# Optimization experiments

Hardware: AMD Instinct MI355X
Metric: run time of the kernel (lower is better)

Reference implementation:

```python
import jax, jax.numpy as jnp
import numpy as np

N = 55          # node count hardcoded in the original forward's reshape
IN_CH = 8192    # in_channel
OUT_SZ = 8192   # out_sz
NEG_SLOPE = 0.01  # torch nn.LeakyReLU default


def setup_inputs() -> dict:
    key = jax.random.key(0)
    ks = jax.random.split(key, 8)
    s1 = 1.0 / np.sqrt(IN_CH)
    s2 = 1.0 / np.sqrt(OUT_SZ)
    return {
        "x": jax.random.normal(ks[0], (N, IN_CH), dtype=jnp.float32),
        "adj": jax.random.uniform(ks[1], (N, N), dtype=jnp.float32),       # unused by forward
        "p_covs": jax.random.uniform(ks[2], (N,), dtype=jnp.float32),      # unused by forward
        # conv1: Conv1d(in_channel, out_sz, 1) == per-node linear
        "W1": jax.random.uniform(ks[3], (OUT_SZ, IN_CH), jnp.float32, -s1, s1),
        "b1": jax.random.uniform(ks[4], (OUT_SZ,), jnp.float32, -s1, s1),
        # conv2_1 / conv2_2: Conv1d(out_sz, 1, 1) == dot with vector + scalar bias
        "a1": jax.random.uniform(ks[5], (OUT_SZ,), jnp.float32, -s2, s2),
        "ba1": jnp.zeros((), jnp.float32),
        "a2": jax.random.uniform(ks[6], (OUT_SZ,), jnp.float32, -s2, s2),
        "ba2": jnp.zeros((), jnp.float32),
    }


def reference(x, adj, p_covs, W1, b1, a1, ba1, a2, ba2):
    # seq_fts = conv1(x.reshape([55, in_channel, 1])) -> [N, out_sz] (len-1 spatial dim squeezed)
    seq_fts = x @ W1.T + b1                        # [N, O]
    # f_1, f_2: 1-channel 1x1 convs -> per-node scalars
    f1 = seq_fts @ a1 + ba1                        # [N]
    f2 = seq_fts @ a2 + ba2                        # [N]
    # logits = f_1 + transpose(f_2, 2, 1): both [N,1,1] -> elementwise per-node scalar
    logits = jax.nn.leaky_relu(f1 + f2, NEG_SLOPE)  # [N]
    # softmax over dim=1, which has size 1 -> coefs are all ones (faithful to source)
    coefs = jax.nn.softmax(logits[:, None, None], axis=1)  # [N,1,1]
    # ret = matmul(coefs, seq_fts^T)^T -> per-node scale of seq_fts
    ret = coefs[:, 0, 0][:, None] * seq_fts        # [N, O]
    # dropout layers are treated as identity (eval mode / p-drop inactive for determinism)
    out = jax.nn.elu(ret)[:, :, None]              # [N, O, 1], matching torch output shape
    return out
```

## Files before the change

kernel.cpp:

```cpp
#include <hip/hip_runtime.h>
#include <hip/hip_bf16.h>
#include <math.h>

#define NN 55
#define KK 8192
#define OO 8192

using bf16x8 = __attribute__((ext_vector_type(8))) __bf16;
using f32x4  = __attribute__((ext_vector_type(4))) float;

__device__ inline bf16x8 cvt8(f32x4 lo, f32x4 hi) {
    bf16x8 v;
    v[0] = (__bf16)lo[0]; v[1] = (__bf16)lo[1];
    v[2] = (__bf16)lo[2]; v[3] = (__bf16)lo[3];
    v[4] = (__bf16)hi[0]; v[5] = (__bf16)hi[1];
    v[6] = (__bf16)hi[2]; v[7] = (__bf16)hi[3];
    return v;
}

__global__ __launch_bounds__(256)
void cvt_x(const float* __restrict__ xg, __bf16* __restrict__ xb) {
    const int idx = blockIdx.x * 256 + threadIdx.x;
    const int row = idx >> 10;
    const int c8  = (idx & 1023) * 8;
    bf16x8 v = {};
    if (row < NN) {
        const float* p = xg + (size_t)row * KK + c8;
        v = cvt8(*(const f32x4*)p, *(const f32x4*)(p + 4));
    }
    *(bf16x8*)(xb + (size_t)row * KK + c8) = v;
}

__global__ __launch_bounds__(512, 4)
void gat_gemm_elu2(const __bf16* __restrict__ xb,
                   const float* __restrict__ wg,
                   const float* __restrict__ bg,
                   float* __restrict__ outg) {
    __shared__ float lds[8 * 2048];

    const int tid  = threadIdx.x;
    const int lane = tid & 63;
    const int w    = tid >> 6;
    const int r    = lane & 15;
    const int q    = lane >> 4;

    const int obase = blockIdx.x * 32;
    const int kb0   = w * 1024 + q * 8;

    const float* wp0 = wg + (size_t)(obase + r) * KK + kb0;
    const float* wp1 = wp0 + (size_t)16 * KK;
    const __bf16* ap = xb + (size_t)r * KK + kb0;

    f32x4 acc0[4] = {};
    f32x4 acc1[4] = {};

    f32x4 cw0 = *(const f32x4*)(wp0);
    f32x4 cw1 = *(const f32x4*)(wp0 + 4);
    f32x4 cw2 = *(const f32x4*)(wp1);
    f32x4 cw3 = *(const f32x4*)(wp1 + 4);
    bf16x8 ca0 = *(const bf16x8*)(ap);
    bf16x8 ca1 = *(const bf16x8*)(ap + (size_t)16 * KK);
    bf16x8 ca2 = *(const bf16x8*)(ap + (size_t)32 * KK);
    bf16x8 ca3 = *(const bf16x8*)(ap + (size_t)48 * KK);

    for (int s = 0; s < 32; ++s) {
        const int sn = (s + 1) & 31;
        const f32x4 nw0 = *(const f32x4*)(wp0 + sn * 32);
        const f32x4 nw1 = *(const f32x4*)(wp0 + sn * 32 + 4);
        const f32x4 nw2 = *(const f32x4*)(wp1 + sn * 32);
        const f32x4 nw3 = *(const f32x4*)(wp1 + sn * 32 + 4);
        const bf16x8 na0 = *(const bf16x8*)(ap + sn * 32);
        const bf16x8 na1 = *(const bf16x8*)(ap + (size_t)16 * KK + sn * 32);
        const bf16x8 na2 = *(const bf16x8*)(ap + (size_t)32 * KK + sn * 32);
        const bf16x8 na3 = *(const bf16x8*)(ap + (size_t)48 * KK + sn * 32);

        const bf16x8 b0 = cvt8(cw0, cw1);
        const bf16x8 b1 = cvt8(cw2, cw3);
        acc0[0] = __builtin_amdgcn_mfma_f32_16x16x32_bf16(ca0, b0, acc0[0], 0, 0, 0);
        acc1[0] = __builtin_amdgcn_mfma_f32_16x16x32_bf16(ca0, b1, acc1[0], 0, 0, 0);
        acc0[1] = __builtin_amdgcn_mfma_f32_16x16x32_bf16(ca1, b0, acc0[1], 0, 0, 0);
        acc1[1] = __builtin_amdgcn_mfma_f32_16x16x32_bf16(ca1, b1, acc1[1], 0, 0, 0);
        acc0[2] = __builtin_amdgcn_mfma_f32_16x16x32_bf16(ca2, b0, acc0[2], 0, 0, 0);
        acc1[2] = __builtin_amdgcn_mfma_f32_16x16x32_bf16(ca2, b1, acc1[2], 0, 0, 0);
        acc0[3] = __builtin_amdgcn_mfma_f32_16x16x32_bf16(ca3, b0, acc0[3], 0, 0, 0);
        acc1[3] = __builtin_amdgcn_mfma_f32_16x16x32_bf16(ca3, b1, acc1[3], 0, 0, 0);

        cw0 = nw0; cw1 = nw1; cw2 = nw2; cw3 = nw3;
        ca0 = na0; ca1 = na1; ca2 = na2; ca3 = na3;
    }

#pragma unroll
    for (int mt = 0; mt < 4; ++mt) {
#pragma unroll
        for (int e = 0; e < 4; ++e) {
            const int row = mt * 16 + q * 4 + e;
            lds[w * 2048 + row * 32 + r]      = acc0[mt][e];
            lds[w * 2048 + row * 32 + 16 + r] = acc1[mt][e];
        }
    }
    __syncthreads();

    for (int i = tid; i < 2048; i += 512) {
        float s = 0.f;
#pragma unroll
        for (int ww = 0; ww < 8; ++ww) s += lds[ww * 2048 + i];
        const int row = i >> 5;
        const int col = i & 31;
        const float v = s + bg[obase + col];
        const float res = (v > 0.f) ? v : expm1f(v);
        if (row < NN) outg[(size_t)row * OO + obase + col] = res;
    }
}

extern "C" void kernel_launch(void* const* d_in, const int* in_sizes, int n_in,
                              void* d_out, int out_size, void* d_ws, size_t ws_size,
                              hipStream_t stream) {
    const float* x  = (const float*)d_in[0];
    const float* W1 = (const float*)d_in[3];
    const float* b1 = (const float*)d_in[4];
    float* out = (float*)d_out;
    __bf16* xb = (__bf16*)d_ws;

    cvt_x<<<dim3(256), dim3(256), 0, stream>>>(x, xb);
    gat_gemm_elu2<<<dim3(OO / 32), dim3(512), 0, stream>>>(xb, W1, b1, out);
}
```

Measured before the change: 77.65 us.

## Stage W tiles through LDS with async global_load_lds and 4-deep pipeline

Replaces direct per-thread register loads of fp32 W with asynchronous global-to-LDS copies into a 4-buffer ring. Each k-stage now covers 256 contiguous columns per row, giving fully coalesced row-wise fetches, and an XOR swizzle is meant to avoid LDS bank conflicts. A loads are prefetched three stages ahead to keep more bytes in flight for this bandwidth-bound GEMV-like GEMM. LDS use rises to 128KB, occupancy drops to 2 blocks/CU, and a barrier is added per stage.

```diff
diff --git a/kernel.cpp b/kernel.cpp
--- a/kernel.cpp
+++ b/kernel.cpp
@@ -31,85 +31,121 @@
     *(bf16x8*)(xb + (size_t)row * KK + c8) = v;
 }
 
-__global__ __launch_bounds__(512, 4)
-void gat_gemm_elu2(const __bf16* __restrict__ xb,
+__device__ inline void gll16(const float* src, float* dstLds) {
+    __builtin_amdgcn_global_load_lds(
+        (const __attribute__((address_space(1))) void*)src,
+        (__attribute__((address_space(3))) void*)dstLds, 16, 0, 0);
+}
+
+#define WAITVM(N) asm volatile("s_waitcnt vmcnt(" #N ")" ::: "memory")
+#define BAR() __builtin_amdgcn_s_barrier()
+
+__global__ __launch_bounds__(512, 2)
+void gat_gemm_elu3(const __bf16* __restrict__ xb,
                    const float* __restrict__ wg,
                    const float* __restrict__ bg,
                    float* __restrict__ outg) {
-    __shared__ float lds[8 * 2048];
+    __shared__ float Wbuf[4 * 8192];
 
     const int tid  = threadIdx.x;
     const int lane = tid & 63;
     const int w    = tid >> 6;
     const int r    = lane & 15;
     const int q    = lane >> 4;
+    const int w4   = w * 4;
+    const int obase = blockIdx.x * 32;
 
-    const int obase = blockIdx.x * 32;
-    const int kb0   = w * 1024 + q * 8;
+    const float* wsrc[4];
+#pragma unroll
+    for (int j = 0; j < 4; ++j) {
+        const int lr = w4 + j;
+        wsrc[j] = wg + (size_t)(obase + lr) * KK + ((lane ^ (lr & 7)) << 2);
+    }
+    const __bf16* abase = xb + (size_t)r * KK + w * 32 + q * 8;
 
-    const float* wp0 = wg + (size_t)(obase + r) * KK + kb0;
-    const float* wp1 = wp0 + (size_t)16 * KK;
-    const __bf16* ap = xb + (size_t)r * KK + kb0;
+    const int sw  = (r & 7) << 4;
+    const int kx0 = (w * 128 + q * 32) ^ sw;
+    const int kx1 = (w * 128 + q * 32 + 16) ^ sw;
 
     f32x4 acc0[4] = {};
     f32x4 acc1[4] = {};
+    bf16x8 A0[4], A1[4], A2[4], A3[4];
 
-    f32x4 cw0 = *(const f32x4*)(wp0);
-    f32x4 cw1 = *(const f32x4*)(wp0 + 4);
-    f32x4 cw2 = *(const f32x4*)(wp1);
-    f32x4 cw3 = *(const f32x4*)(wp1 + 4);
-    bf16x8 ca0 = *(const bf16x8*)(ap);
-    bf16x8 ca1 = *(const bf16x8*)(ap + (size_t)16 * KK);
-    bf16x8 ca2 = *(const bf16x8*)(ap + (size_t)32 * KK);
-    bf16x8 ca3 = *(const bf16x8*)(ap + (size_t)48 * KK);
+#define STAGE_W(BUF, STG) do {                                              \
+    const int kb_ = (STG) * 256;                                            \
+    _Pragma("unroll")                                                       \
+    for (int j = 0; j < 4; ++j) {                                           \
+        gll16(wsrc[j] + kb_, &Wbuf[(BUF) * 8192 + (w4 + j) * 256]);         \
+    } } while (0)
 
-    for (int s = 0; s < 32; ++s) {
-        const int sn = (s + 1) & 31;
-        const f32x4 nw0 = *(const f32x4*)(wp0 + sn * 32);
-        const f32x4 nw1 = *(const f32x4*)(wp0 + sn * 32 + 4);
-        const f32x4 nw2 = *(const f32x4*)(wp1 + sn * 32);
-        const f32x4 nw3 = *(const f32x4*)(wp1 + sn * 32 + 4);
-        const bf16x8 na0 = *(const bf16x8*)(ap + sn * 32);
-        const bf16x8 na1 = *(const bf16x8*)(ap + (size_t)16 * KK + sn * 32);
-        const bf16x8 na2 = *(const bf16x8*)(ap + (size_t)32 * KK + sn * 32);
-        const bf16x8 na3 = *(const bf16x8*)(ap + (size_t)48 * KK + sn * 32);
+#define LOAD_A(SLOT, STG) do {                                              \
+    const __bf16* a_ = abase + (size_t)(STG) * 256;                         \
+    SLOT[0] = *(const bf16x8*)(a_);                                         \
+    SLOT[1] = *(const bf16x8*)(a_ + (size_t)16 * KK);                       \
+    SLOT[2] = *(const bf16x8*)(a_ + (size_t)32 * KK);                       \
+    SLOT[3] = *(const bf16x8*)(a_ + (size_t)48 * KK); } while (0)
 
-        const bf16x8 b0 = cvt8(cw0, cw1);
-        const bf16x8 b1 = cvt8(cw2, cw3);
-        acc0[0] = __builtin_amdgcn_mfma_f32_16x16x32_bf16(ca0, b0, acc0[0], 0, 0, 0);
-        acc1[0] = __builtin_amdgcn_mfma_f32_16x16x32_bf16(ca0, b1, acc1[0], 0, 0, 0);
-        acc0[1] = __builtin_amdgcn_mfma_f32_16x16x32_bf16(ca1, b0, acc0[1], 0, 0, 0);
-        acc1[1] = __builtin_amdgcn_mfma_f32_16x16x32_bf16(ca1, b1, acc1[1], 0, 0, 0);
-        acc0[2] = __builtin_amdgcn_mfma_f32_16x16x32_bf16(ca2, b0, acc0[2], 0, 0, 0);
-        acc1[2] = __builtin_amdgcn_mfma_f32_16x16x32_bf16(ca2, b1, acc1[2], 0, 0, 0);
-        acc0[3] = __builtin_amdgcn_mfma_f32_16x16x32_bf16(ca3, b0, acc0[3], 0, 0, 0);
-        acc1[3] = __builtin_amdgcn_mfma_f32_16x16x32_bf16(ca3, b1, acc1[3], 0, 0, 0);
+#define COMPUTE(BUF, AS) do {                                               \
+    const char* wb_ = (const char*)&Wbuf[(BUF) * 8192];                     \
+    const f32x4 lo0 = *(const f32x4*)(wb_ + r * 1024 + kx0);                \
+    const f32x4 hi0 = *(const f32x4*)(wb_ + r * 1024 + kx1);                \
+    const f32x4 lo1 = *(const f32x4*)(wb_ + (16 + r) * 1024 + kx0);         \
+    const f32x4 hi1 = *(const f32x4*)(wb_ + (16 + r) * 1024 + kx1);         \
+    const bf16x8 b0 = cvt8(lo0, hi0);                                       \
+    const bf16x8 b1 = cvt8(lo1, hi1);                                       \
+    acc0[0] = __builtin_amdgcn_mfma_f32_16x16x32_bf16(AS[0], b0, acc0[0], 0, 0, 0); \
+    acc1[0] = __builtin_amdgcn_mfma_f32_16x16x32_bf16(AS[0], b1, acc1[0], 0, 0, 0); \
+    acc0[1] = __builtin_amdgcn_mfma_f32_16x16x32_bf16(AS[1], b0, acc0[1], 0, 0, 0); \
+    acc1[1] = __builtin_amdgcn_mfma_f32_16x16x32_bf16(AS[1], b1, acc1[1], 0, 0, 0); \
+    acc0[2] = __builtin_amdgcn_mfma_f32_16x16x32_bf16(AS[2], b0, acc0[2], 0, 0, 0); \
+    acc1[2] = __builtin_amdgcn_mfma_f32_16x16x32_bf16(AS[2], b1, acc1[2], 0, 0, 0); \
+    acc0[3] = __builtin_amdgcn_mfma_f32_16x16x32_bf16(AS[3], b0, acc0[3], 0, 0, 0); \
+    acc1[3] = __builtin_amdgcn_mfma_f32_16x16x32_bf16(AS[3], b1, acc1[3], 0, 0, 0); \
+    } while (0)
 
-        cw0 = nw0; cw1 = nw1; cw2 = nw2; cw3 = nw3;
-        ca0 = na0; ca1 = na1; ca2 = na2; ca3 = na3;
+    STAGE_W(0, 0); LOAD_A(A0, 0);
+    STAGE_W(1, 1); LOAD_A(A1, 1);
+    STAGE_W(2, 2); LOAD_A(A2, 2);
+
+    int s = 0;
+#pragma unroll 1
+    for (int su = 0; su < 7; ++su) {
+        WAITVM(16); BAR(); STAGE_W(3, s + 3); LOAD_A(A3, s + 3); COMPUTE(0, A0);
+        WAITVM(16); BAR(); STAGE_W(0, s + 4); LOAD_A(A0, s + 4); COMPUTE(1, A1);
+        WAITVM(16); BAR(); STAGE_W(1, s + 5); LOAD_A(A1, s + 5); COMPUTE(2, A2);
+        WAITVM(16); BAR(); STAGE_W(2, s + 6); LOAD_A(A2, s + 6); COMPUTE(3, A3);
+        s += 4;
     }
+    WAITVM(16); BAR(); STAGE_W(3, 31); LOAD_A(A3, 31); COMPUTE(0, A0);
+    WAITVM(16); BAR(); COMPUTE(1, A1);
+    WAITVM(8);  BAR(); COMPUTE(2, A2);
+    WAITVM(0);  BAR(); COMPUTE(3, A3);
 
+    float* red = Wbuf;
 #pragma unroll
     for (int mt = 0; mt < 4; ++mt) {
 #pragma unroll
         for (int e = 0; e < 4; ++e) {
             const int row = mt * 16 + q * 4 + e;
-            lds[w * 2048 + row * 32 + r]      = acc0[mt][e];
-            lds[w * 2048 + row * 32 + 16 + r] = acc1[mt][e];
+            red[w * 2048 + row * 32 + r]      = acc0[mt][e];
+            red[w * 2048 + row * 32 + 16 + r] = acc1[mt][e];
         }
     }
     __syncthreads();
 
     for (int i = tid; i < 2048; i += 512) {
-        float s = 0.f;
+        float ssum = 0.f;
 #pragma unroll
-        for (int ww = 0; ww < 8; ++ww) s += lds[ww * 2048 + i];
+        for (int ww = 0; ww < 8; ++ww) ssum += red[ww * 2048 + i];
         const int row = i >> 5;
         const int col = i & 31;
-        const float v = s + bg[obase + col];
+        const float v = ssum + bg[obase + col];
         const float res = (v > 0.f) ? v : expm1f(v);
         if (row < NN) outg[(size_t)row * OO + obase + col] = res;
     }
+#undef STAGE_W
+#undef LOAD_A
+#undef COMPUTE
 }
 
 extern "C" void kernel_launch(void* const* d_in, const int* in_sizes, int n_in,
@@ -122,5 +158,5 @@
     __bf16* xb = (__bf16*)d_ws;
 
     cvt_x<<<dim3(256), dim3(256), 0, stream>>>(x, xb);
-    gat_gemm_elu2<<<dim3(OO / 32), dim3(512), 0, stream>>>(xb, W1, b1, out);
+    gat_gemm_elu3<<<dim3(OO / 32), dim3(512), 0, stream>>>(xb, W1, b1, out);
 }
```

Measured after the change: 62.64 us. 1.24x faster.

## Deepen GEMM load pipeline to four register slots with explicit vmcnt waits

Applied to the files above, without the earlier changes.

Replaces the one-step register prefetch in the bf16 MFMA GEMM with a four-slot ring of in-flight global loads, three steps ahead, using manual s_waitcnt vmcnt to wait only on the oldest slot. The goal is more memory-level parallelism on the fp32 weight stream, which dominates this memory-bound kernel. Launch bounds drop from 4 to 2 blocks per SIMD group to leave room for the extra live registers, so occupancy falls in exchange for deeper per-wave prefetch. The hand-written vmcnt counts rely on the compiler emitting loads exactly in the expected order.

```diff
diff --git a/kernel.cpp b/kernel.cpp
--- a/kernel.cpp
+++ b/kernel.cpp
@@ -31,85 +31,103 @@
     *(bf16x8*)(xb + (size_t)row * KK + c8) = v;
 }
 
-__global__ __launch_bounds__(512, 4)
-void gat_gemm_elu2(const __bf16* __restrict__ xb,
-                   const float* __restrict__ wg,
-                   const float* __restrict__ bg,
-                   float* __restrict__ outg) {
-    __shared__ float lds[8 * 2048];
+#define WAITVM(N) asm volatile("s_waitcnt vmcnt(" #N ")" ::: "memory")
+
+struct WSlot { f32x4 a, b, c, d; };
+struct ASlot { bf16x8 a, b, c, d; };
+
+__global__ __launch_bounds__(512, 2)
+void gat_gemm_elu11(const __bf16* __restrict__ xb,
+                    const float* __restrict__ wg,
+                    const float* __restrict__ bg,
+                    float* __restrict__ outg) {
+    __shared__ float red[8 * 2048];
 
     const int tid  = threadIdx.x;
     const int lane = tid & 63;
     const int w    = tid >> 6;
     const int r    = lane & 15;
     const int q    = lane >> 4;
+    const int obase = blockIdx.x * 32;
 
-    const int obase = blockIdx.x * 32;
-    const int kb0   = w * 1024 + q * 8;
-
-    const float* wp0 = wg + (size_t)(obase + r) * KK + kb0;
-    const float* wp1 = wp0 + (size_t)16 * KK;
-    const __bf16* ap = xb + (size_t)r * KK + kb0;
+    const int kb = w * 1024 + q * 8;
+    const float*  wp0 = wg + (size_t)(obase + r) * KK + kb;
+    const float*  wp1 = wp0 + (size_t)16 * KK;
+    const __bf16* ap0 = xb + (size_t)r * KK + kb;
+    const __bf16* ap1 = ap0 + (size_t)16 * KK;
+    const __bf16* ap2 = ap0 + (size_t)32 * KK;
+    const __bf16* ap3 = ap0 + (size_t)48 * KK;
 
     f32x4 acc0[4] = {};
     f32x4 acc1[4] = {};
+    WSlot w0, w1, w2, w3;
+    ASlot a0, a1, a2, a3;
 
-    f32x4 cw0 = *(const f32x4*)(wp0);
-    f32x4 cw1 = *(const f32x4*)(wp0 + 4);
-    f32x4 cw2 = *(const f32x4*)(wp1);
-    f32x4 cw3 = *(const f32x4*)(wp1 + 4);
-    bf16x8 ca0 = *(const bf16x8*)(ap);
-    bf16x8 ca1 = *(const bf16x8*)(ap + (size_t)16 * KK);
-    bf16x8 ca2 = *(const bf16x8*)(ap + (size_t)32 * KK);
-    bf16x8 ca3 = *(const bf16x8*)(ap + (size_t)48 * KK);
+#define ISSUE(WS, AS, JW) do {                                               \
+    WS.a = *(const f32x4*) ((const char*)wp0 + (JW) * 128);                  \
+    WS.b = *(const f32x4*) ((const char*)wp0 + (JW) * 128 + 16);             \
+    WS.c = *(const f32x4*) ((const char*)wp1 + (JW) * 128);                  \
+    WS.d = *(const f32x4*) ((const char*)wp1 + (JW) * 128 + 16);             \
+    AS.a = *(const bf16x8*)((const char*)ap0 + (JW) * 64);                   \
+    AS.b = *(const bf16x8*)((const char*)ap1 + (JW) * 64);                   \
+    AS.c = *(const bf16x8*)((const char*)ap2 + (JW) * 64);                   \
+    AS.d = *(const bf16x8*)((const char*)ap3 + (JW) * 64);                   \
+} while (0)
 
-    for (int s = 0; s < 32; ++s) {
-        const int sn = (s + 1) & 31;
-        const f32x4 nw0 = *(const f32x4*)(wp0 + sn * 32);
-        const f32x4 nw1 = *(const f32x4*)(wp0 + sn * 32 + 4);
-        const f32x4 nw2 = *(const f32x4*)(wp1 + sn * 32);
-        const f32x4 nw3 = *(const f32x4*)(wp1 + sn * 32 + 4);
-        const bf16x8 na0 = *(const bf16x8*)(ap + sn * 32);
-        const bf16x8 na1 = *(const bf16x8*)(ap + (size_t)16 * KK + sn * 32);
-        const bf16x8 na2 = *(const bf16x8*)(ap + (size_t)32 * KK + sn * 32);
-        const bf16x8 na3 = *(const bf16x8*)(ap + (size_t)48 * KK + sn * 32);
+#define COMP(WS, AS) do {                                                    \
+    const bf16x8 b0 = cvt8(WS.a, WS.b);                                      \
+    const bf16x8 b1 = cvt8(WS.c, WS.d);                                      \
+    acc0[0] = __builtin_amdgcn_mfma_f32_16x16x32_bf16(AS.a, b0, acc0[0], 0, 0, 0); \
+    acc1[0] = __builtin_amdgcn_mfma_f32_16x16x32_bf16(AS.a, b1, acc1[0], 0, 0, 0); \
+    acc0[1] = __builtin_amdgcn_mfma_f32_16x16x32_bf16(AS.b, b0, acc0[1], 0, 0, 0); \
+    acc1[1] = __builtin_amdgcn_mfma_f32_16x16x32_bf16(AS.b, b1, acc1[1], 0, 0, 0); \
+    acc0[2] = __builtin_amdgcn_mfma_f32_16x16x32_bf16(AS.c, b0, acc0[2], 0, 0, 0); \
+    acc1[2] = __builtin_amdgcn_mfma_f32_16x16x32_bf16(AS.c, b1, acc1[2], 0, 0, 0); \
+    acc0[3] = __builtin_amdgcn_mfma_f32_16x16x32_bf16(AS.d, b0, acc0[3], 0, 0, 0); \
+    acc1[3] = __builtin_amdgcn_mfma_f32_16x16x32_bf16(AS.d, b1, acc1[3], 0, 0, 0); \
+} while (0)
 
-        const bf16x8 b0 = cvt8(cw0, cw1);
-        const bf16x8 b1 = cvt8(cw2, cw3);
-        acc0[0] = __builtin_amdgcn_mfma_f32_16x16x32_bf16(ca0, b0, acc0[0], 0, 0, 0);
-        acc1[0] = __builtin_amdgcn_mfma_f32_16x16x32_bf16(ca0, b1, acc1[0], 0, 0, 0);
-        acc0[1] = __builtin_amdgcn_mfma_f32_16x16x32_bf16(ca1, b0, acc0[1], 0, 0, 0);
-        acc1[1] = __builtin_amdgcn_mfma_f32_16x16x32_bf16(ca1, b1, acc1[1], 0, 0, 0);
-        acc0[2] = __builtin_amdgcn_mfma_f32_16x16x32_bf16(ca2, b0, acc0[2], 0, 0, 0);
-        acc1[2] = __builtin_amdgcn_mfma_f32_16x16x32_bf16(ca2, b1, acc1[2], 0, 0, 0);
-        acc0[3] = __builtin_amdgcn_mfma_f32_16x16x32_bf16(ca3, b0, acc0[3], 0, 0, 0);
-        acc1[3] = __builtin_amdgcn_mfma_f32_16x16x32_bf16(ca3, b1, acc1[3], 0, 0, 0);
+    ISSUE(w0, a0, 0);
+    ISSUE(w1, a1, 1);
+    ISSUE(w2, a2, 2);
 
-        cw0 = nw0; cw1 = nw1; cw2 = nw2; cw3 = nw3;
-        ca0 = na0; ca1 = na1; ca2 = na2; ca3 = na3;
+#pragma unroll 1
+    for (int g = 0; g < 7; ++g) {
+        WAITVM(16); COMP(w0, a0); ISSUE(w3, a3, 3);
+        WAITVM(16); COMP(w1, a1); ISSUE(w0, a0, 4);
+        WAITVM(16); COMP(w2, a2); ISSUE(w1, a1, 5);
+        WAITVM(16); COMP(w3, a3); ISSUE(w2, a2, 6);
+        wp0 += 128; wp1 += 128;
+        ap0 += 128; ap1 += 128; ap2 += 128; ap3 += 128;
     }
+    WAITVM(16); COMP(w0, a0); ISSUE(w3, a3, 3);
+    WAITVM(16); COMP(w1, a1);
+    WAITVM(8);  COMP(w2, a2);
+    WAITVM(0);  COMP(w3, a3);
 
 #pragma unroll
     for (int mt = 0; mt < 4; ++mt) {
 #pragma unroll
         for (int e = 0; e < 4; ++e) {
             const int row = mt * 16 + q * 4 + e;
-            lds[w * 2048 + row * 32 + r]      = acc0[mt][e];
-            lds[w * 2048 + row * 32 + 16 + r] = acc1[mt][e];
+            red[w * 2048 + row * 32 + r]      = acc0[mt][e];
+            red[w * 2048 + row * 32 + 16 + r] = acc1[mt][e];
         }
     }
     __syncthreads();
 
     for (int i = tid; i < 2048; i += 512) {
-        float s = 0.f;
+        float ssum = 0.f;
 #pragma unroll
-        for (int ww = 0; ww < 8; ++ww) s += lds[ww * 2048 + i];
+        for (int ww = 0; ww < 8; ++ww) ssum += red[ww * 2048 + i];
         const int row = i >> 5;
         const int col = i & 31;
-        const float v = s + bg[obase + col];
+        const float v = ssum + bg[obase + col];
         const float res = (v > 0.f) ? v : expm1f(v);
         if (row < NN) outg[(size_t)row * OO + obase + col] = res;
     }
+#undef ISSUE
+#undef COMP
 }
 
 extern "C" void kernel_launch(void* const* d_in, const int* in_sizes, int n_in,
@@ -122,5 +140,5 @@
     __bf16* xb = (__bf16*)d_ws;
 
     cvt_x<<<dim3(256), dim3(256), 0, stream>>>(x, xb);
-    gat_gemm_elu2<<<dim3(OO / 32), dim3(512), 0, stream>>>(xb, W1, b1, out);
+    gat_gemm_elu11<<<dim3(OO / 32), dim3(512), 0, stream>>>(xb, W1, b1, out);
 }
```

After: 76.15 us. About the same (-1.9%).
